# Kernel tuning notes

Hardware: AMD Instinct MI355X
Metric: run time of the kernel (lower is better)

The kernel has to match this reference:

```python
import jax, jax.numpy as jnp
import numpy as np

N = 512            # n_inputs (even)
L = N              # n_layers = n_inputs
PE = N // 2        # couplers per even column
PO = N // 2 - 1    # couplers per odd column
TWO_PI = 6.283185307179586


def _ste_clamp(theta):
    # clamp_ste: clamp value to [0, 2*pi], straight-through gradient
    c = jnp.clip(theta, 0.0, TWO_PI)
    return theta + jax.lax.stop_gradient(c - theta)


def _phase(theta):
    return jax.lax.complex(jnp.cos(theta), jnp.sin(theta))


def _pc_even(M, theta):
    # phase shifter on upper arm of each even pair: rows 0,2,4,...
    return M.at[0::2].multiply(_phase(theta)[:, None])


def _pc_odd(M, theta):
    # phase shifter on upper arm of each odd pair: rows 1,3,...,N-3
    return M.at[1:N - 1:2].multiply(_phase(theta)[:, None])


def _mmi_coeffs(loss, imb):
    # lossy, imbalanced 2x2 MMI: a*[[t, i r],[i r, t]]
    a = jnp.sqrt(1.0 - loss)
    t = a * jnp.sqrt(0.5 + imb)
    r = a * jnp.sqrt(0.5 - imb)
    ir = jax.lax.complex(jnp.zeros_like(r), r)
    return t, ir


def _mmi_even(M, loss, imb):
    t, ir = _mmi_coeffs(loss, imb)
    Mp = M.reshape(PE, 2, N)                       # pairs (0,1),(2,3),...
    top, bot = Mp[:, 0], Mp[:, 1]
    nt = t[:, None] * top + ir[:, None] * bot
    nb = ir[:, None] * top + t[:, None] * bot
    return jnp.stack([nt, nb], axis=1).reshape(N, N)


def _mmi_odd(M, loss, imb):
    t, ir = _mmi_coeffs(loss, imb)
    Mi = M[1:N - 1].reshape(PO, 2, N)              # pairs (1,2),(3,4),...
    top, bot = Mi[:, 0], Mi[:, 1]
    nt = t[:, None] * top + ir[:, None] * bot
    nb = ir[:, None] * top + t[:, None] * bot
    mid = jnp.stack([nt, nb], axis=1).reshape(N - 2, N)
    return jnp.concatenate([M[:1], mid, M[N - 1:]], axis=0)


def _forward(pc_even_phases, pc_odd_phases, pc_out_phases,
             mmi_loss_even, mmi_imb_even, mmi_loss_odd, mmi_imb_odd):
    pe = _ste_clamp(pc_even_phases).reshape(L // 2, 2, PE)
    po = _ste_clamp(pc_odd_phases).reshape(L // 2, 2, PO)
    le = mmi_loss_even.reshape(L // 2, 2, PE)
    ie = mmi_imb_even.reshape(L // 2, 2, PE)
    lo = mmi_loss_odd.reshape(L // 2, 2, PO)
    io = mmi_imb_odd.reshape(L // 2, 2, PO)

    def step(M, p):
        pe_, le_, ie_, po_, lo_, io_ = p
        for j in range(2):  # two even PC+MMI columns
            M = _pc_even(M, pe_[j])
            M = _mmi_even(M, le_[j], ie_[j])
        for j in range(2):  # two odd PC+MMI columns
            M = _pc_odd(M, po_[j])
            M = _mmi_odd(M, lo_[j], io_[j])
        return M, None

    M0 = jnp.eye(N, dtype=jnp.complex64)
    M, _ = jax.lax.scan(jax.checkpoint(step), M0, (pe, le, ie, po, lo, io))
    # output phase column on every wire
    return M * _phase(_ste_clamp(pc_out_phases))[:, None]


def setup_inputs() -> dict:
    key = jax.random.key(0)
    ks = jax.random.split(key, 7)
    return {
        "pc_even_phases": jax.random.uniform(ks[0], (L, PE), jnp.float32, 0.0, TWO_PI),
        "pc_odd_phases": jax.random.uniform(ks[1], (L, PO), jnp.float32, 0.0, TWO_PI),
        "pc_out_phases": jax.random.uniform(ks[2], (N,), jnp.float32, 0.0, TWO_PI),
        "mmi_loss_even": jax.random.uniform(ks[3], (L, PE), jnp.float32, 0.0, 0.05),
        "mmi_imb_even": jax.random.uniform(ks[4], (L, PE), jnp.float32, -0.05, 0.05),
        "mmi_loss_odd": jax.random.uniform(ks[5], (L, PO), jnp.float32, 0.0, 0.05),
        "mmi_imb_odd": jax.random.uniform(ks[6], (L, PO), jnp.float32, -0.05, 0.05),
    }


def reference(pc_even_phases, pc_odd_phases, pc_out_phases,
              mmi_loss_even, mmi_imb_even, mmi_loss_odd, mmi_imb_odd):
    return _forward(pc_even_phases, pc_odd_phases, pc_out_phases,
                    mmi_loss_even, mmi_imb_even, mmi_loss_odd, mmi_imb_odd)
```

## Files before the change

kernel.cpp:

```cpp
#include <hip/hip_runtime.h>
#include <hip/hip_fp16.h>

#define TWO_PI_F 6.283185307179586f

__device__ __forceinline__ float clamp02pi(float x) {
    return fminf(fmaxf(x, 0.0f), TWO_PI_F);
}

__device__ __forceinline__ float2 cmul(const float2 a, const float2 b) {
    return make_float2(a.x * b.x - a.y * b.y, a.x * b.y + a.y * b.x);
}
__device__ __forceinline__ float2 cadd(const float2 a, const float2 b) {
    return make_float2(a.x + b.x, a.y + b.y);
}
__device__ __forceinline__ float2 cscale(const float s, const float2 a) {
    return make_float2(s * a.x, s * a.y);
}
__device__ __forceinline__ float2 imul(const float r, const float2 e) {
    return make_float2(-r * e.y, r * e.x);
}
__device__ __forceinline__ float2 cfma(const float2 acc, const float2 a, const float2 b) {
    return make_float2(acc.x + a.x * b.x - a.y * b.y,
                       acc.y + a.x * b.y + a.y * b.x);
}

__device__ __forceinline__ float2 h2f(const unsigned u) {
    return __half22float2(__builtin_bit_cast(__half2, u));
}
__device__ __forceinline__ unsigned f2h(const float2 f) {
    return __builtin_bit_cast(unsigned, __float22half2_rn(f));
}

__device__ __forceinline__ void compose_row_w(
    const float4 (*sE)[72], const float4 (*sO)[72], const int r, const int P0,
    float4& h0, float4& h1)
{
    float2 f0, f1, f2, f3;
    if (r == 0) {
        const float4 q1 = sE[1][0], q0 = sE[0][0];
        const float2 e1 = make_float2(q1.x, q1.y);
        const float2 e0 = make_float2(q0.x, q0.y);
        const float2 v2 = cscale(q1.z, e1);
        const float2 v3 = make_float2(0.0f, q1.w);
        f2 = cadd(cmul(v2, cscale(q0.z, e0)), cmul(v3, imul(q0.w, e0)));
        f3 = cadd(cmul(v2, make_float2(0.0f, q0.w)), cscale(q0.z, v3));
        f0 = make_float2(0.0f, 0.0f);
        f1 = make_float2(0.0f, 0.0f);
    } else {
        const int pidx = ((r - 1) >> 1) - P0;
        const int qidx = min(((r - 1) >> 1) + 1, 255) - P0;
        const float4 qO1 = sO[1][pidx], qO0 = sO[0][pidx];
        const float2 eO1 = make_float2(qO1.x, qO1.y);
        const float2 eO0 = make_float2(qO0.x, qO0.y);
        float2 w1, w2;
        if (r & 1) { w1 = cscale(qO1.z, eO1); w2 = make_float2(0.0f, qO1.w); }
        else       { w1 = imul(qO1.w, eO1);   w2 = make_float2(qO1.z, 0.0f); }
        const float2 u1 = cadd(cmul(w1, cscale(qO0.z, eO0)),
                               cmul(w2, imul(qO0.w, eO0)));
        const float2 u2 = cadd(cmul(w1, make_float2(0.0f, qO0.w)),
                               cscale(qO0.z, w2));
        const float4 qE1p = sE[1][pidx], qE1q = sE[1][qidx];
        const float4 qE0p = sE[0][pidx], qE0q = sE[0][qidx];
        const float2 eE1p = make_float2(qE1p.x, qE1p.y);
        const float2 eE1q = make_float2(qE1q.x, qE1q.y);
        const float2 eE0p = make_float2(qE0p.x, qE0p.y);
        const float2 eE0q = make_float2(qE0q.x, qE0q.y);
        const float2 v0 = cmul(u1, imul(qE1p.w, eE1p));
        const float2 v1 = cscale(qE1p.z, u1);
        const float2 v2 = cmul(u2, cscale(qE1q.z, eE1q));
        const float2 v3 = cmul(u2, make_float2(0.0f, qE1q.w));
        f0 = cadd(cmul(v0, cscale(qE0p.z, eE0p)), cmul(v1, imul(qE0p.w, eE0p)));
        f1 = cadd(cmul(v0, make_float2(0.0f, qE0p.w)), cscale(qE0p.z, v1));
        f2 = cadd(cmul(v2, cscale(qE0q.z, eE0q)), cmul(v3, imul(qE0q.w, eE0q)));
        f3 = cadd(cmul(v2, make_float2(0.0f, qE0q.w)), cscale(qE0q.z, v3));
    }
    h0 = make_float4(f0.x, f0.y, f1.x, f1.y);
    h1 = make_float4(f2.x, f2.y, f3.x, f3.y);
}

__global__ __launch_bounds__(256) void compose8q_kernel(
    const float* __restrict__ pe, const float* __restrict__ po,
    const float* __restrict__ le, const float* __restrict__ ie,
    const float* __restrict__ lo, const float* __restrict__ io,
    uint4* __restrict__ Mch8)
{
    const int q = blockIdx.x;
    const int j = q >> 2;
    const int quarter = q & 3;
    const int R0 = 128 * quarter;
    const int P0 = (quarter == 0) ? 0 : ((R0 - 3) >> 1);
    const int t = threadIdx.x;

    __shared__ float4 sE[4][72];
    __shared__ float4 sO[4][72];
    __shared__ float4 B4[2][134][2];

    for (int it = t; it < 576; it += 256) {
        const int half = it / 288;
        const int rem  = it % 288;
        const int sub  = rem / 72;
        const int w    = rem % 72;
        const int p    = P0 + w;
        if (p > 255) continue;
        if (half == 0) {
            const int idx = (4 * j + sub) * 256 + p;
            float s, c;
            __sincosf(clamp02pi(pe[idx]), &s, &c);
            const float a = sqrtf(1.0f - le[idx]);
            sE[sub][w] = make_float4(c, s, a * sqrtf(0.5f + ie[idx]),
                                           a * sqrtf(0.5f - ie[idx]));
        } else {
            float4 qv = make_float4(1.0f, 0.0f, 1.0f, 0.0f);
            if (p < 255) {
                const int odx = (4 * j + sub) * 255 + p;
                float s, c;
                __sincosf(clamp02pi(po[odx]), &s, &c);
                const float a = sqrtf(1.0f - lo[odx]);
                qv = make_float4(c, s, a * sqrtf(0.5f + io[odx]),
                                       a * sqrtf(0.5f - io[odx]));
            }
            sO[sub][w] = qv;
        }
    }
    __syncthreads();

    for (int it = t; it < 268; it += 256) {
        const int s = it / 134, slot = it % 134;
        const int row = R0 - 2 + slot;
        if (row >= 0 && row <= 511) {
            float4 h0, h1;
            compose_row_w(&sE[2 * s], &sO[2 * s], row, P0, h0, h1);
            B4[s][slot][0] = h0;
            B4[s][slot][1] = h1;
        }
    }
    __syncthreads();

    if (t < 128) {
        const int r = R0 + t;
        const int base = (r & 1) ? (r - 1) : (r - 2);
        const int sr = t + 2;
        const float4 wv0 = B4[1][sr][0], wv1 = B4[1][sr][1];
        const float2 w0 = make_float2(wv0.x, wv0.y), w1 = make_float2(wv0.z, wv0.w);
        const float2 w2 = make_float2(wv1.x, wv1.y), w3 = make_float2(wv1.z, wv1.w);
        float2 p0 = make_float2(0.f,0.f), p1 = p0, p2 = p0, p3 = p0,
               p4 = p0, p5 = p0, p6 = p0, p7 = p0;
        {   const int k = min(max(base, 0), 511) - (R0 - 2);
            const float4 a = B4[0][k][0], b = B4[0][k][1];
            p0 = cfma(p0, w0, make_float2(a.x, a.y));
            p1 = cfma(p1, w0, make_float2(a.z, a.w));
            p2 = cfma(p2, w0, make_float2(b.x, b.y));
            p3 = cfma(p3, w0, make_float2(b.z, b.w)); }
        {   const int k = min(max(base + 1, 0), 511) - (R0 - 2);
            const float4 a = B4[0][k][0], b = B4[0][k][1];
            p2 = cfma(p2, w1, make_float2(a.x, a.y));
            p3 = cfma(p3, w1, make_float2(a.z, a.w));
            p4 = cfma(p4, w1, make_float2(b.x, b.y));
            p5 = cfma(p5, w1, make_float2(b.z, b.w)); }
        {   const int k = min(max(base + 2, 0), 511) - (R0 - 2);
            const float4 a = B4[0][k][0], b = B4[0][k][1];
            p2 = cfma(p2, w2, make_float2(a.x, a.y));
            p3 = cfma(p3, w2, make_float2(a.z, a.w));
            p4 = cfma(p4, w2, make_float2(b.x, b.y));
            p5 = cfma(p5, w2, make_float2(b.z, b.w)); }
        {   const int k = min(max(base + 3, 0), 511) - (R0 - 2);
            const float4 a = B4[0][k][0], b = B4[0][k][1];
            p4 = cfma(p4, w3, make_float2(a.x, a.y));
            p5 = cfma(p5, w3, make_float2(a.z, a.w));
            p6 = cfma(p6, w3, make_float2(b.x, b.y));
            p7 = cfma(p7, w3, make_float2(b.z, b.w)); }
        uint4* dst = Mch8 + (size_t)j * 1024 + r;
        dst[0]   = make_uint4(f2h(p0), f2h(p1), f2h(p2), f2h(p3));
        dst[512] = make_uint4(f2h(p4), f2h(p5), f2h(p6), f2h(p7));
    }
}

__device__ __forceinline__ float2 hrow4(const uint4 q, const float2 a,
                                        const float2 b, const float2 d,
                                        const float2 e, float2 acc)
{
    acc = cfma(acc, h2f(q.x), a);
    acc = cfma(acc, h2f(q.y), b);
    acc = cfma(acc, h2f(q.z), d);
    acc = cfma(acc, h2f(q.w), e);
    return acc;
}

__global__ __launch_bounds__(256) void mesh8p_kernel(
    const uint4* __restrict__ Mch,
    const float* __restrict__ pout,
    float* __restrict__ out, const int out_size)
{
    const int t   = threadIdx.x;
    const int col = blockIdx.x;
    const int r0  = 2 * t, r1 = r0 + 1;

    __shared__ float4 S[2][264];

    float2 Y0 = make_float2((r0 == col) ? 1.0f : 0.0f, 0.0f);
    float2 Y1 = make_float2((r1 == col) ? 1.0f : 0.0f, 0.0f);
    S[0][t + 2] = make_float4(Y0.x, Y0.y, Y1.x, Y1.y);
    if (t < 2) {
        const float4 z = make_float4(0.f, 0.f, 0.f, 0.f);
        S[0][t] = z; S[1][t] = z;
        S[0][258 + t] = z; S[1][258 + t] = z;
    }

    uint4 c0e = Mch[r0], c1e = Mch[512 + r0];
    uint4 c0o = Mch[r1], c1o = Mch[512 + r1];
    __syncthreads();

#pragma unroll 1
    for (int i = 0; i < 128; ++i) {
        const int nb = ((i + 1) & 127) * 1024;
        const uint4 n0e = Mch[nb + r0], n1e = Mch[nb + 512 + r0];
        const uint4 n0o = Mch[nb + r1], n1o = Mch[nb + 512 + r1];

        const float4* SS = S[i & 1];
        const float4 q0 = SS[t],     q1 = SS[t + 1], q2 = SS[t + 2],
                     q3 = SS[t + 3], q4 = SS[t + 4];

        Y0 = hrow4(c0e, make_float2(q0.x, q0.y), make_float2(q0.z, q0.w),
                        make_float2(q1.x, q1.y), make_float2(q1.z, q1.w),
                   make_float2(0.f, 0.f));
        Y0 = hrow4(c1e, make_float2(q2.x, q2.y), make_float2(q2.z, q2.w),
                        make_float2(q3.x, q3.y), make_float2(q3.z, q3.w), Y0);

        Y1 = hrow4(c0o, make_float2(q1.x, q1.y), make_float2(q1.z, q1.w),
                        make_float2(q2.x, q2.y), make_float2(q2.z, q2.w),
                   make_float2(0.f, 0.f));
        Y1 = hrow4(c1o, make_float2(q3.x, q3.y), make_float2(q3.z, q3.w),
                        make_float2(q4.x, q4.y), make_float2(q4.z, q4.w), Y1);

        S[(i + 1) & 1][t + 2] = make_float4(Y0.x, Y0.y, Y1.x, Y1.y);
        __syncthreads();

        c0e = n0e; c1e = n1e; c0o = n0o; c1o = n1o;
    }

    float s0, cc0, s1, cc1;
    __sincosf(clamp02pi(pout[r0]), &s0, &cc0);
    __sincosf(clamp02pi(pout[r1]), &s1, &cc1);
    const int o0 = r0 * 512 + col;
    const int o1 = r1 * 512 + col;
    if (o0 < out_size) out[o0] = cc0 * Y0.x - s0 * Y0.y;
    if (o1 < out_size) out[o1] = cc1 * Y1.x - s1 * Y1.y;
}

__global__ __launch_bounds__(256) void mesh_kernel(
    const float* __restrict__ pe, const float* __restrict__ po,
    const float* __restrict__ pout,
    const float* __restrict__ le, const float* __restrict__ ie,
    const float* __restrict__ lo, const float* __restrict__ io,
    float* __restrict__ out, const int out_size)
{
    const int p = threadIdx.x;
    const int b = blockIdx.x;

    __shared__ float4 P[2][256];

    P[0][p] = (p == b) ? make_float4(1.0f, 0.0f, 0.0f, 0.0f)
                       : make_float4(0.0f, 0.0f, 0.0f, 0.0f);
    P[1][p] = (p == b) ? make_float4(0.0f, 0.0f, 1.0f, 0.0f)
                       : make_float4(0.0f, 0.0f, 0.0f, 0.0f);

#pragma unroll 1
    for (int i = 0; i < 256; ++i) {
        const int e0 = (2 * i) * 256 + p, e1 = e0 + 256;
        const float pe0 = pe[e0], le0 = le[e0], ie0 = ie[e0];
        const float pe1 = pe[e1], le1 = le[e1], ie1 = ie[e1];
        float po0 = 0.0f, lo0 = 0.0f, io0 = 0.0f;
        float po1 = 0.0f, lo1 = 0.0f, io1 = 0.0f;
        if (p < 255) {
            const int o0 = (2 * i) * 255 + p, o1 = o0 + 255;
            po0 = po[o0]; lo0 = lo[o0]; io0 = io[o0];
            po1 = po[o1]; lo1 = lo[o1]; io1 = io[o1];
        }

        float4 v0 = P[0][p];
        float4 v1 = P[1][p];
#pragma unroll
        for (int j = 0; j < 2; ++j) {
            float s, c;
            __sincosf(clamp02pi(j ? pe1 : pe0), &s, &c);
            const float a  = sqrtf(1.0f - (j ? le1 : le0));
            const float tt = a * sqrtf(0.5f + (j ? ie1 : ie0));
            const float rr = a * sqrtf(0.5f - (j ? ie1 : ie0));
            {
                const float ptr_ = c * v0.x - s * v0.y;
                const float pti_ = c * v0.y + s * v0.x;
                v0 = make_float4(tt * ptr_ - rr * v0.w, tt * pti_ + rr * v0.z,
                                 tt * v0.z - rr * pti_, tt * v0.w + rr * ptr_);
            }
            {
                const float ptr_ = c * v1.x - s * v1.y;
                const float pti_ = c * v1.y + s * v1.x;
                v1 = make_float4(tt * ptr_ - rr * v1.w, tt * pti_ + rr * v1.z,
                                 tt * v1.z - rr * pti_, tt * v1.w + rr * ptr_);
            }
        }
        P[0][p] = v0;
        P[1][p] = v1;
        __syncthreads();

        if (p < 255) {
            float2 top0 = make_float2(P[0][p].z, P[0][p].w);
            float2 bot0 = make_float2(P[0][p + 1].x, P[0][p + 1].y);
            float2 top1 = make_float2(P[1][p].z, P[1][p].w);
            float2 bot1 = make_float2(P[1][p + 1].x, P[1][p + 1].y);
#pragma unroll
            for (int j = 0; j < 2; ++j) {
                float s, c;
                __sincosf(clamp02pi(j ? po1 : po0), &s, &c);
                const float a  = sqrtf(1.0f - (j ? lo1 : lo0));
                const float tt = a * sqrtf(0.5f + (j ? io1 : io0));
                const float rr = a * sqrtf(0.5f - (j ? io1 : io0));
                {
                    const float ptr_ = c * top0.x - s * top0.y;
                    const float pti_ = c * top0.y + s * top0.x;
                    const float nbx = tt * bot0.x - rr * pti_;
                    const float nby = tt * bot0.y + rr * ptr_;
                    top0 = make_float2(tt * ptr_ - rr * bot0.y, tt * pti_ + rr * bot0.x);
                    bot0 = make_float2(nbx, nby);
                }
                {
                    const float ptr_ = c * top1.x - s * top1.y;
                    const float pti_ = c * top1.y + s * top1.x;
                    const float nbx = tt * bot1.x - rr * pti_;
                    const float nby = tt * bot1.y + rr * ptr_;
                    top1 = make_float2(tt * ptr_ - rr * bot1.y, tt * pti_ + rr * bot1.x);
                    bot1 = make_float2(nbx, nby);
                }
            }
            P[0][p].z = top0.x; P[0][p].w = top0.y;
            P[0][p + 1].x = bot0.x; P[0][p + 1].y = bot0.y;
            P[1][p].z = top1.x; P[1][p].w = top1.y;
            P[1][p + 1].x = bot1.x; P[1][p + 1].y = bot1.y;
        }
        __syncthreads();
    }

    const float4 v0 = P[0][p];
    const float4 v1 = P[1][p];
    float s0, c0, s1, c1;
    __sincosf(clamp02pi(pout[2 * p]),     &s0, &c0);
    __sincosf(clamp02pi(pout[2 * p + 1]), &s1, &c1);

    float4 w0, w1;
    w0.x = c0 * v0.x - s0 * v0.y;  w0.y = c0 * v0.y + s0 * v0.x;
    w0.z = c0 * v1.x - s0 * v1.y;  w0.w = c0 * v1.y + s0 * v1.x;
    w1.x = c1 * v0.z - s1 * v0.w;  w1.y = c1 * v0.w + s1 * v0.z;
    w1.z = c1 * v1.z - s1 * v1.w;  w1.w = c1 * v1.w + s1 * v1.z;

    const int i0 = (2 * p) * 512 + 2 * b;
    const int i1 = (2 * p + 1) * 512 + 2 * b;
    if (i0 + 1 < out_size) *(float2*)(out + i0) = make_float2(w0.x, w0.z);
    if (i1 + 1 < out_size) *(float2*)(out + i1) = make_float2(w1.x, w1.z);
}

extern "C" void kernel_launch(void* const* d_in, const int* in_sizes, int n_in,
                              void* d_out, int out_size, void* d_ws, size_t ws_size,
                              hipStream_t stream)
{
    const float* pe   = (const float*)d_in[0];
    const float* po   = (const float*)d_in[1];
    const float* pout = (const float*)d_in[2];
    const float* le   = (const float*)d_in[3];
    const float* ie   = (const float*)d_in[4];
    const float* lo   = (const float*)d_in[5];
    const float* io   = (const float*)d_in[6];

    const size_t need = (size_t)128 * 1024 * sizeof(uint4);
    if (ws_size >= need) {
        uint4* Mch8 = (uint4*)d_ws;
        compose8q_kernel<<<512, 256, 0, stream>>>(pe, po, le, ie, lo, io, Mch8);
        mesh8p_kernel<<<512, 256, 0, stream>>>(Mch8, pout, (float*)d_out, out_size);
    } else {
        mesh_kernel<<<256, 256, 0, stream>>>(pe, po, pout, le, ie, lo, io,
                                             (float*)d_out, out_size);
    }
}
```

Measured before the change: 139.2 us.

## Process two identity columns per block to reuse decoded mesh coefficients

The mesh application kernel now propagates two input columns per block instead of one, halving the grid to 256 blocks. Each thread decodes its half-precision coefficients once and applies them to both columns, so global coefficient loads and conversions are shared across the pair, and outputs are written as float2. In exchange, register and shared-memory use per block rise, and with half as many blocks fewer CUs may be busy on the 256-CU-class device. The serial chain of 128 synchronised steps per block is unchanged.

```diff
diff --git a/kernel.cpp b/kernel.cpp
--- a/kernel.cpp
+++ b/kernel.cpp
@@ -175,35 +175,45 @@
     }
 }
 
-__device__ __forceinline__ float2 hrow4(const uint4 q, const float2 a,
-                                        const float2 b, const float2 d,
-                                        const float2 e, float2 acc)
-{
-    acc = cfma(acc, h2f(q.x), a);
-    acc = cfma(acc, h2f(q.y), b);
-    acc = cfma(acc, h2f(q.z), d);
-    acc = cfma(acc, h2f(q.w), e);
+__device__ __forceinline__ float2 row8(
+    const float2 k0, const float2 k1, const float2 k2, const float2 k3,
+    const float2 k4, const float2 k5, const float2 k6, const float2 k7,
+    const float4 w0, const float4 w1, const float4 w2, const float4 w3)
+{
+    float2 acc = make_float2(0.f, 0.f);
+    acc = cfma(acc, k0, make_float2(w0.x, w0.y));
+    acc = cfma(acc, k1, make_float2(w0.z, w0.w));
+    acc = cfma(acc, k2, make_float2(w1.x, w1.y));
+    acc = cfma(acc, k3, make_float2(w1.z, w1.w));
+    acc = cfma(acc, k4, make_float2(w2.x, w2.y));
+    acc = cfma(acc, k5, make_float2(w2.z, w2.w));
+    acc = cfma(acc, k6, make_float2(w3.x, w3.y));
+    acc = cfma(acc, k7, make_float2(w3.z, w3.w));
     return acc;
 }
 
-__global__ __launch_bounds__(256) void mesh8p_kernel(
+__global__ __launch_bounds__(256) void mesh8d_kernel(
     const uint4* __restrict__ Mch,
     const float* __restrict__ pout,
     float* __restrict__ out, const int out_size)
 {
-    const int t   = threadIdx.x;
-    const int col = blockIdx.x;
-    const int r0  = 2 * t, r1 = r0 + 1;
-
-    __shared__ float4 S[2][264];
-
-    float2 Y0 = make_float2((r0 == col) ? 1.0f : 0.0f, 0.0f);
-    float2 Y1 = make_float2((r1 == col) ? 1.0f : 0.0f, 0.0f);
-    S[0][t + 2] = make_float4(Y0.x, Y0.y, Y1.x, Y1.y);
+    const int t    = threadIdx.x;
+    const int colA = blockIdx.x * 2;
+    const int r0   = 2 * t, r1 = r0 + 1;
+
+    __shared__ float4 SA[2][264];
+    __shared__ float4 SB[2][264];
+
+    float2 YA0 = make_float2((r0 == colA)     ? 1.0f : 0.0f, 0.0f);
+    float2 YA1 = make_float2((r1 == colA)     ? 1.0f : 0.0f, 0.0f);
+    float2 YB0 = make_float2((r0 == colA + 1) ? 1.0f : 0.0f, 0.0f);
+    float2 YB1 = make_float2((r1 == colA + 1) ? 1.0f : 0.0f, 0.0f);
+    SA[0][t + 2] = make_float4(YA0.x, YA0.y, YA1.x, YA1.y);
+    SB[0][t + 2] = make_float4(YB0.x, YB0.y, YB1.x, YB1.y);
     if (t < 2) {
         const float4 z = make_float4(0.f, 0.f, 0.f, 0.f);
-        S[0][t] = z; S[1][t] = z;
-        S[0][258 + t] = z; S[1][258 + t] = z;
+        SA[0][t] = z; SA[1][t] = z; SA[0][258 + t] = z; SA[1][258 + t] = z;
+        SB[0][t] = z; SB[1][t] = z; SB[0][258 + t] = z; SB[1][258 + t] = z;
     }
 
     uint4 c0e = Mch[r0], c1e = Mch[512 + r0];
@@ -216,23 +226,29 @@
         const uint4 n0e = Mch[nb + r0], n1e = Mch[nb + 512 + r0];
         const uint4 n0o = Mch[nb + r1], n1o = Mch[nb + 512 + r1];
 
-        const float4* SS = S[i & 1];
-        const float4 q0 = SS[t],     q1 = SS[t + 1], q2 = SS[t + 2],
-                     q3 = SS[t + 3], q4 = SS[t + 4];
-
-        Y0 = hrow4(c0e, make_float2(q0.x, q0.y), make_float2(q0.z, q0.w),
-                        make_float2(q1.x, q1.y), make_float2(q1.z, q1.w),
-                   make_float2(0.f, 0.f));
-        Y0 = hrow4(c1e, make_float2(q2.x, q2.y), make_float2(q2.z, q2.w),
-                        make_float2(q3.x, q3.y), make_float2(q3.z, q3.w), Y0);
-
-        Y1 = hrow4(c0o, make_float2(q1.x, q1.y), make_float2(q1.z, q1.w),
-                        make_float2(q2.x, q2.y), make_float2(q2.z, q2.w),
-                   make_float2(0.f, 0.f));
-        Y1 = hrow4(c1o, make_float2(q3.x, q3.y), make_float2(q3.z, q3.w),
-                        make_float2(q4.x, q4.y), make_float2(q4.z, q4.w), Y1);
-
-        S[(i + 1) & 1][t + 2] = make_float4(Y0.x, Y0.y, Y1.x, Y1.y);
+        const float4* A = SA[i & 1];
+        const float4* B = SB[i & 1];
+        const float4 a0 = A[t],     a1 = A[t + 1], a2 = A[t + 2],
+                     a3 = A[t + 3], a4 = A[t + 4];
+        const float4 b0 = B[t],     b1 = B[t + 1], b2 = B[t + 2],
+                     b3 = B[t + 3], b4 = B[t + 4];
+
+        const float2 k0 = h2f(c0e.x), k1 = h2f(c0e.y),
+                     k2 = h2f(c0e.z), k3 = h2f(c0e.w);
+        const float2 k4 = h2f(c1e.x), k5 = h2f(c1e.y),
+                     k6 = h2f(c1e.z), k7 = h2f(c1e.w);
+        const float2 m0 = h2f(c0o.x), m1 = h2f(c0o.y),
+                     m2 = h2f(c0o.z), m3 = h2f(c0o.w);
+        const float2 m4 = h2f(c1o.x), m5 = h2f(c1o.y),
+                     m6 = h2f(c1o.z), m7 = h2f(c1o.w);
+
+        YA0 = row8(k0, k1, k2, k3, k4, k5, k6, k7, a0, a1, a2, a3);
+        YA1 = row8(m0, m1, m2, m3, m4, m5, m6, m7, a1, a2, a3, a4);
+        YB0 = row8(k0, k1, k2, k3, k4, k5, k6, k7, b0, b1, b2, b3);
+        YB1 = row8(m0, m1, m2, m3, m4, m5, m6, m7, b1, b2, b3, b4);
+
+        SA[(i + 1) & 1][t + 2] = make_float4(YA0.x, YA0.y, YA1.x, YA1.y);
+        SB[(i + 1) & 1][t + 2] = make_float4(YB0.x, YB0.y, YB1.x, YB1.y);
         __syncthreads();
 
         c0e = n0e; c1e = n1e; c0o = n0o; c1o = n1o;
@@ -241,10 +257,14 @@
     float s0, cc0, s1, cc1;
     __sincosf(clamp02pi(pout[r0]), &s0, &cc0);
     __sincosf(clamp02pi(pout[r1]), &s1, &cc1);
-    const int o0 = r0 * 512 + col;
-    const int o1 = r1 * 512 + col;
-    if (o0 < out_size) out[o0] = cc0 * Y0.x - s0 * Y0.y;
-    if (o1 < out_size) out[o1] = cc1 * Y1.x - s1 * Y1.y;
+    const int o0 = r0 * 512 + colA;
+    const int o1 = r1 * 512 + colA;
+    if (o0 + 1 < out_size)
+        *(float2*)(out + o0) = make_float2(cc0 * YA0.x - s0 * YA0.y,
+                                           cc0 * YB0.x - s0 * YB0.y);
+    if (o1 + 1 < out_size)
+        *(float2*)(out + o1) = make_float2(cc1 * YA1.x - s1 * YA1.y,
+                                           cc1 * YB1.x - s1 * YB1.y);
 }
 
 __global__ __launch_bounds__(256) void mesh_kernel(
@@ -374,7 +394,7 @@
     if (ws_size >= need) {
         uint4* Mch8 = (uint4*)d_ws;
         compose8q_kernel<<<512, 256, 0, stream>>>(pe, po, le, ie, lo, io, Mch8);
-        mesh8p_kernel<<<512, 256, 0, stream>>>(Mch8, pout, (float*)d_out, out_size);
+        mesh8d_kernel<<<256, 256, 0, stream>>>(Mch8, pout, (float*)d_out, out_size);
     } else {
         mesh_kernel<<<256, 256, 0, stream>>>(pe, po, pout, le, ie, lo, io,
                                              (float*)d_out, out_size);
```

After: 156.2 us. 12.2% more time.
